# Optimization experiments

Hardware: AMD Instinct MI355X
Metric: run time of the kernel (lower is better)

The kernel has to match this reference:

```python
import jax, jax.numpy as jnp
import numpy as np

# 8 sign-flip operations: all combinations of (+-1, +-1, +-1), shape [8, 3]
OPS = jnp.array([[i, j, k] for i in (-1, 1) for j in (-1, 1) for k in (-1, 1)],
                dtype=jnp.float32)


def setup_inputs() -> dict:
    key = jax.random.key(0)
    k1, k2 = jax.random.split(key)
    B, N = 256, 4096
    X = jax.random.normal(k1, (B, N, 3), dtype=jnp.float32)
    mask = jnp.ones((B, N), dtype=jnp.float32)
    return {"X": X, "mask": mask}


def reference(X, mask):
    # X: [B, N, 3], mask: [B, N]
    m = mask[..., None]                                   # [B, N, 1]
    center = (X * m).sum(axis=1) / m.sum(axis=1)          # [B, 3]
    # torch: X = X - center.unsqueeze(1) * mask  (subtract center only where masked)
    Xc = X - center[:, None, :] * m                       # [B, N, 3]
    # 3x3 covariance per batch element
    C = jnp.einsum('bpi,bpj->bij', Xc, Xc)                # [B, 3, 3]
    # eigh on detached covariance (no grad through eigendecomposition)
    L, V = jnp.linalg.eigh(jax.lax.stop_gradient(C))      # V: [B, 3, 3]
    # F_ops[b,o,i,j] = ops[o,j] * V[b,i,j]  -> [B, 8, 3, 3]
    F_ops = OPS[None, :, None, :] * V[:, None, :, :]
    # h[b,o,p,i] = sum_j F_ops[b,o,j,i] * Xc[b,p,j]
    h = jnp.einsum('boji,bpj->bopi', F_ops, Xc)           # [B, 8, N, 3]
    h = h.reshape(X.shape[0] * 8, X.shape[1], 3)          # [B*8, N, 3]
    return h, jax.lax.stop_gradient(F_ops), center
```

## Files before the change

kernel.cpp:

```cpp
#include <hip/hip_runtime.h>
#include <math.h>

#ifndef USE_NEW_LARTG
#define USE_NEW_LARTG 1
#endif

#define BB 256
#define NN 4096


__device__ __forceinline__ float ssign_(float a, float b) {
  return (b >= 0.0f) ? fabsf(a) : -fabsf(a);
}

__device__ __forceinline__ float slapy2f_(float x, float y) {
#pragma clang fp contract(off)
  float xa = fabsf(x), ya = fabsf(y);
  float w = fmaxf(xa, ya), z = fminf(xa, ya);
  if (z == 0.0f) return w;
  float q = z / w;
  return w * __fsqrt_rn(1.0f + q * q);
}

__device__ __forceinline__ void slartgf_(float f, float g, float& cs, float& sn, float& r) {
#pragma clang fp contract(off)
#if USE_NEW_LARTG
  if (g == 0.0f) { cs = 1.0f; sn = 0.0f; r = f; }
  else if (f == 0.0f) { cs = 0.0f; sn = (g >= 0.0f) ? 1.0f : -1.0f; r = fabsf(g); }
  else {
    float d = __fsqrt_rn(f * f + g * g);
    cs = fabsf(f) / d;
    r = ssign_(d, f);
    sn = g / r;
  }
#else
  if (g == 0.0f) { cs = 1.0f; sn = 0.0f; r = f; }
  else if (f == 0.0f) { cs = 0.0f; sn = 1.0f; r = g; }
  else {
    float rr = __fsqrt_rn(f * f + g * g);
    cs = f / rr;
    sn = g / rr;
    r = rr;
    if (fabsf(f) > fabsf(g) && cs < 0.0f) { cs = -cs; sn = -sn; r = -r; }
  }
#endif
}

__device__ void slaev2f_(float a, float b, float c, float& rt1, float& rt2,
                         float& cs1, float& sn1) {
#pragma clang fp contract(off)
  float sm = a + c;
  float df = a - c;
  float adf = fabsf(df);
  float tb = b + b;
  float ab = fabsf(tb);
  float acmx, acmn;
  if (fabsf(a) > fabsf(c)) { acmx = a; acmn = c; } else { acmx = c; acmn = a; }
  float rt;
  if (adf > ab)      { float q = ab / adf; rt = adf * __fsqrt_rn(1.0f + q * q); }
  else if (adf < ab) { float q = adf / ab; rt = ab * __fsqrt_rn(1.0f + q * q); }
  else               { rt = ab * __fsqrt_rn(2.0f); }
  int sgn1;
  if (sm < 0.0f)      { rt1 = 0.5f * (sm - rt); sgn1 = -1; rt2 = (acmx / rt1) * acmn - (b / rt1) * b; }
  else if (sm > 0.0f) { rt1 = 0.5f * (sm + rt); sgn1 = 1;  rt2 = (acmx / rt1) * acmn - (b / rt1) * b; }
  else                { rt1 = 0.5f * rt; rt2 = -0.5f * rt; sgn1 = 1; }
  float cs;
  int sgn2;
  if (df >= 0.0f) { cs = df + rt; sgn2 = 1; } else { cs = df - rt; sgn2 = -1; }
  float acs = fabsf(cs);
  if (acs > ab) {
    float ct = -tb / cs;
    sn1 = 1.0f / __fsqrt_rn(1.0f + ct * ct);
    cs1 = ct * sn1;
  } else {
    if (ab == 0.0f) { cs1 = 1.0f; sn1 = 0.0f; }
    else { float tn = -cs / tb; cs1 = 1.0f / __fsqrt_rn(1.0f + tn * tn); sn1 = tn * cs1; }
  }
  if (sgn1 == sgn2) { float tn = cs1; cs1 = -sn1; sn1 = tn; }
}

__device__ void steqr3f_(float* d, float* e, float z[4][4]) {
#pragma clang fp contract(off)
  const float eps = 5.9604645e-08f;
  const float eps2 = eps * eps;
  const float safmin = 1.17549435e-38f;
  const int n = 3, nm1 = 2, nmaxit = 3 * 30;
  int jtot = 0, l1 = 1;
  int l, m, lsv, lend, lendsv, i, j, ii, k;
  float p, g, r, c, s, f, b, rt1, rt2, tst, anorm, temp, cj, sj;
  float wc[3], ws_[3];
  wc[0] = wc[1] = wc[2] = 0.0f; ws_[0] = ws_[1] = ws_[2] = 0.0f;

L10:
  if (l1 > n) goto L160;
  if (l1 > 1) e[l1 - 1] = 0.0f;
  if (l1 <= nm1) {
    for (m = l1; m <= nm1; ++m) {
      tst = fabsf(e[m]);
      if (tst == 0.0f) goto L30;
      if (tst <= (__fsqrt_rn(fabsf(d[m])) * __fsqrt_rn(fabsf(d[m + 1]))) * eps) {
        e[m] = 0.0f; goto L30;
      }
    }
  }
  m = n;
L30:
  l = l1; lsv = l; lend = m; lendsv = lend; l1 = m + 1;
  if (lend == l) goto L10;
  anorm = 0.0f;
  for (i = l; i <= lend; ++i) anorm = fmaxf(anorm, fabsf(d[i]));
  for (i = l; i <= lend - 1; ++i) anorm = fmaxf(anorm, fabsf(e[i]));
  if (anorm == 0.0f) goto L10;
  if (fabsf(d[lend]) < fabsf(d[l])) { lend = lsv; l = lendsv; }

  if (lend > l) {
L40:
    if (l != lend) {
      for (m = l; m <= lend - 1; ++m) {
        tst = e[m] * e[m];
        if (tst <= (eps2 * fabsf(d[m])) * fabsf(d[m + 1]) + safmin) goto L60;
      }
    }
    m = lend;
L60:
    if (m < lend) e[m] = 0.0f;
    p = d[l];
    if (m == l) goto L80;
    if (m == l + 1) {
      slaev2f_(d[l], e[l], d[l + 1], rt1, rt2, c, s);
      wc[l] = c; ws_[l] = s;
      for (i = 1; i <= 3; ++i) {
        temp = z[i][l + 1];
        z[i][l + 1] = c * temp - s * z[i][l];
        z[i][l]     = s * temp + c * z[i][l];
      }
      d[l] = rt1; d[l + 1] = rt2; e[l] = 0.0f;
      l = l + 2;
      if (l <= lend) goto L40;
      goto L140;
    }
    if (jtot == nmaxit) goto L140;
    jtot = jtot + 1;
    g = (d[l + 1] - p) / (2.0f * e[l]);
    r = slapy2f_(g, 1.0f);
    g = d[m] - p + e[l] / (g + ssign_(r, g));
    s = 1.0f; c = 1.0f; p = 0.0f;
    for (i = m - 1; i >= l; --i) {
      f = s * e[i]; b = c * e[i];
      slartgf_(g, f, c, s, r);
      if (i != m - 1) e[i + 1] = r;
      g = d[i + 1] - p;
      r = (d[i] - g) * s + 2.0f * c * b;
      p = s * r;
      d[i + 1] = g + p;
      g = c * r - b;
      wc[i] = c; ws_[i] = -s;
    }
    for (j = (m - l + 1) - 1; j >= 1; --j) {
      cj = wc[l + j - 1]; sj = ws_[l + j - 1];
      for (i = 1; i <= 3; ++i) {
        temp = z[i][l + j];
        z[i][l + j]     = cj * temp - sj * z[i][l + j - 1];
        z[i][l + j - 1] = sj * temp + cj * z[i][l + j - 1];
      }
    }
    d[l] = d[l] - p;
    e[l] = g;
    goto L40;
L80:
    d[l] = p;
    l = l + 1;
    if (l <= lend) goto L40;
    goto L140;
  } else {
L90:
    if (l != lend) {
      for (m = l; m >= lend + 1; --m) {
        tst = e[m - 1] * e[m - 1];
        if (tst <= (eps2 * fabsf(d[m])) * fabsf(d[m - 1]) + safmin) goto L110;
      }
    }
    m = lend;
L110:
    if (m > lend) e[m - 1] = 0.0f;
    p = d[l];
    if (m == l) goto L130;
    if (m == l - 1) {
      slaev2f_(d[l - 1], e[l - 1], d[l], rt1, rt2, c, s);
      wc[m] = c; ws_[m] = s;
      for (i = 1; i <= 3; ++i) {
        temp = z[i][l];
        z[i][l]     = c * temp - s * z[i][l - 1];
        z[i][l - 1] = s * temp + c * z[i][l - 1];
      }
      d[l - 1] = rt1; d[l] = rt2; e[l - 1] = 0.0f;
      l = l - 2;
      if (l >= lend) goto L90;
      goto L140;
    }
    if (jtot == nmaxit) goto L140;
    jtot = jtot + 1;
    g = (d[l - 1] - p) / (2.0f * e[l - 1]);
    r = slapy2f_(g, 1.0f);
    g = d[m] - p + e[l - 1] / (g + ssign_(r, g));
    s = 1.0f; c = 1.0f; p = 0.0f;
    for (i = m; i <= l - 1; ++i) {
      f = s * e[i]; b = c * e[i];
      slartgf_(g, f, c, s, r);
      if (i != m) e[i - 1] = r;
      g = d[i] - p;
      r = (d[i + 1] - g) * s + 2.0f * c * b;
      p = s * r;
      d[i] = g + p;
      g = c * r - b;
      wc[i] = c; ws_[i] = s;
    }
    for (j = 1; j <= (l - m + 1) - 1; ++j) {
      cj = wc[m + j - 1]; sj = ws_[m + j - 1];
      for (i = 1; i <= 3; ++i) {
        temp = z[i][m + j];
        z[i][m + j]     = cj * temp - sj * z[i][m + j - 1];
        z[i][m + j - 1] = sj * temp + cj * z[i][m + j - 1];
      }
    }
    d[l] = d[l] - p;
    e[l - 1] = g;
    goto L90;
L130:
    d[l] = p;
    l = l - 1;
    if (l >= lend) goto L90;
    goto L140;
  }
L140:
  if (jtot < nmaxit) goto L10;
  goto L190;
L160:
  for (ii = 2; ii <= n; ++ii) {
    i = ii - 1; k = i; p = d[i];
    for (j = ii; j <= n; ++j) {
      if (d[j] < p) { k = j; p = d[j]; }
    }
    if (k != i) {
      d[k] = d[i]; d[i] = p;
      for (int q = 1; q <= 3; ++q) { temp = z[q][i]; z[q][i] = z[q][k]; z[q][k] = temp; }
    }
  }
L190:
  return;
}

__device__ void eigh3f_(const float C[3][3], float V[3][3]) {
#pragma clang fp contract(off)
  float a11 = C[0][0], a21 = C[1][0], a31 = C[2][0];
  float a22 = C[1][1], a32 = C[2][1], a33 = C[2][2];
  float d[4], e[3], tau1, v3;
  float xnorm = fabsf(a31);
  if (xnorm == 0.0f) {
    tau1 = 0.0f; v3 = 0.0f;
    d[1] = a11; d[2] = a22; d[3] = a33; e[1] = a21; e[2] = a32;
  } else {
    float beta = -ssign_(slapy2f_(a21, xnorm), a21);
    tau1 = (beta - a21) / beta;
    v3 = a31 / (a21 - beta);
    e[1] = beta;
    float x1 = tau1 * a22 + tau1 * (a32 * v3);
    float x2 = tau1 * a32 + (tau1 * v3) * a33;
    float al = -0.5f * tau1 * (x1 + x2 * v3);
    float w1 = x1 + al;
    float w2 = x2 + al * v3;
    d[1] = a11;
    d[2] = (a22 - w1) - w1;
    e[2] = (a32 - v3 * w1) - w2;
    d[3] = (a33 - v3 * w2) - w2 * v3;
  }
  float z[4][4];
  for (int i = 1; i <= 3; ++i)
    for (int j = 1; j <= 3; ++j) z[i][j] = (i == j) ? 1.0f : 0.0f;
  steqr3f_(d, e, z);
  if (tau1 != 0.0f) {
    for (int j = 1; j <= 3; ++j) {
      float wj = z[2][j] + z[3][j] * v3;
      float tmp = -(tau1 * wj);
      z[2][j] = z[2][j] + tmp;
      z[3][j] = z[3][j] + v3 * tmp;
    }
  }
  for (int i = 0; i < 3; ++i)
    for (int j = 0; j < 3; ++j) V[i][j] = z[i + 1][j + 1];
}

__global__ __launch_bounds__(256) void k_stats_eigh(
    const float* __restrict__ X, const float* __restrict__ mask,
    float* __restrict__ out_fops, float* __restrict__ out_center,
    float* __restrict__ ws) {
  int b = blockIdx.x;
  int t = threadIdx.x;
  const float4* Xv = reinterpret_cast<const float4*>(X);
  const float4* Mv = reinterpret_cast<const float4*>(mask);

  double acc[11];
  for (int q = 0; q < 11; ++q) acc[q] = 0.0;
  for (int kk = 0; kk < 4; ++kk) {
    int fi = b * 3072 + kk * 768 + 3 * t;
    float4 v0 = Xv[fi], v1 = Xv[fi + 1], v2 = Xv[fi + 2];
    float4 mm = Mv[b * 1024 + kk * 256 + t];
    float px[4] = {v0.x, v0.w, v1.z, v2.y};
    float py[4] = {v0.y, v1.x, v1.w, v2.z};
    float pz[4] = {v0.z, v1.y, v2.x, v2.w};
    float pm[4] = {mm.x, mm.y, mm.z, mm.w};
#pragma unroll
    for (int q = 0; q < 4; ++q) {
      double x = px[q], y = py[q], zz = pz[q], m = pm[q];
      acc[0] += m;       acc[1] += m * m;
      acc[2] += m * x;   acc[3] += m * y;   acc[4] += m * zz;
      acc[5] += x * x;   acc[6] += x * y;   acc[7] += x * zz;
      acc[8] += y * y;   acc[9] += y * zz;  acc[10] += zz * zz;
    }
  }
#pragma unroll
  for (int off = 32; off > 0; off >>= 1)
    for (int q = 0; q < 11; ++q) acc[q] += __shfl_down(acc[q], off, 64);

  __shared__ double sh[4][11];
  int wid = t >> 6, lane = t & 63;
  if (lane == 0)
    for (int q = 0; q < 11; ++q) sh[wid][q] = acc[q];
  __syncthreads();

  if (t == 0) {
    double r[11];
    for (int q = 0; q < 11; ++q) r[q] = sh[0][q] + sh[1][q] + sh[2][q] + sh[3][q];
    double W = r[0], W2 = r[1];
    double ssum[3] = {r[2], r[3], r[4]};
    double M[3][3] = {{r[5], r[6], r[7]}, {r[6], r[8], r[9]}, {r[7], r[9], r[10]}};
    double cc[3] = {ssum[0] / W, ssum[1] / W, ssum[2] / W};
    float Cf[3][3];
    for (int i = 0; i < 3; ++i)
      for (int j = 0; j < 3; ++j)
        Cf[i][j] = (float)(M[i][j] - (ssum[i] * cc[j] + cc[i] * ssum[j]) + W2 * cc[i] * cc[j]);
    float Vf[3][3];
    eigh3f_(Cf, Vf);
    float cf[3] = {(float)cc[0], (float)cc[1], (float)cc[2]};
    float* wb = ws + b * 12;
    for (int i = 0; i < 3; ++i)
      for (int j = 0; j < 3; ++j) wb[i * 3 + j] = Vf[i][j];
    wb[9] = cf[0]; wb[10] = cf[1]; wb[11] = cf[2];
    out_center[b * 3 + 0] = cf[0];
    out_center[b * 3 + 1] = cf[1];
    out_center[b * 3 + 2] = cf[2];
    for (int o = 0; o < 8; ++o) {
      float sgn[3] = {(o & 4) ? 1.f : -1.f, (o & 2) ? 1.f : -1.f, (o & 1) ? 1.f : -1.f};
      for (int i = 0; i < 3; ++i)
        for (int j = 0; j < 3; ++j)
          out_fops[b * 72 + o * 9 + i * 3 + j] = sgn[j] * Vf[i][j];
    }
  }
}

__global__ __launch_bounds__(256) void k_apply(
    const float* __restrict__ X, const float* __restrict__ mask,
    const float* __restrict__ ws, float* __restrict__ h) {
  int blk = blockIdx.x;
  int b = blk >> 2;
  int chunk = blk & 3;
  int t = threadIdx.x;

  const float* wb = ws + b * 12;
  float V0 = wb[0], V1 = wb[1], V2 = wb[2];
  float V3 = wb[3], V4 = wb[4], V5 = wb[5];
  float V6 = wb[6], V7 = wb[7], V8 = wb[8];
  float c0 = wb[9], c1 = wb[10], c2 = wb[11];

  const float4* Xv = reinterpret_cast<const float4*>(X);
  int fi = b * 3072 + chunk * 768 + 3 * t;
  float4 v0 = Xv[fi], v1 = Xv[fi + 1], v2 = Xv[fi + 2];
  float4 mm = reinterpret_cast<const float4*>(mask)[b * 1024 + chunk * 256 + t];
  float px[4] = {v0.x, v0.w, v1.z, v2.y};
  float py[4] = {v0.y, v1.x, v1.w, v2.z};
  float pz[4] = {v0.z, v1.y, v2.x, v2.w};
  float pm[4] = {mm.x, mm.y, mm.z, mm.w};

  float ya[4], yb[4], yc[4];
#pragma unroll
  for (int q = 0; q < 4; ++q) {
    float xcx = px[q] - c0 * pm[q];
    float xcy = py[q] - c1 * pm[q];
    float xcz = pz[q] - c2 * pm[q];
    ya[q] = V0 * xcx + V3 * xcy + V6 * xcz;
    yb[q] = V1 * xcx + V4 * xcy + V7 * xcz;
    yc[q] = V2 * xcx + V5 * xcy + V8 * xcz;
  }

  __shared__ float ylds[3072];
  float4* yv = reinterpret_cast<float4*>(ylds);
  yv[3 * t]     = make_float4(ya[0], yb[0], yc[0], ya[1]);
  yv[3 * t + 1] = make_float4(yb[1], yc[1], ya[2], yb[2]);
  yv[3 * t + 2] = make_float4(yc[2], ya[3], yb[3], yc[3]);
  __syncthreads();

  uint4 r0 = reinterpret_cast<const uint4*>(ylds)[t];
  uint4 r1 = reinterpret_cast<const uint4*>(ylds)[t + 256];
  uint4 r2 = reinterpret_cast<const uint4*>(ylds)[t + 512];

  int c0i = t % 3;
  int c1i = c0i + 1; if (c1i == 3) c1i = 0;
  int c2i = c1i + 1; if (c2i == 3) c2i = 0;

  uint4* hv = reinterpret_cast<uint4*>(h);
  int hb = 3072 * (b * 8) + 768 * chunk;
#pragma unroll
  for (int o = 0; o < 8; ++o) {
    unsigned s0 = (o & 4) ? 0u : 0x80000000u;
    unsigned s1 = (o & 2) ? 0u : 0x80000000u;
    unsigned s2 = (o & 1) ? 0u : 0x80000000u;
    unsigned sg[3] = {s0, s1, s2};
    uint4 m0 = make_uint4(sg[c0i], sg[c1i], sg[c2i], sg[c0i]);
    uint4 m1 = make_uint4(sg[c1i], sg[c2i], sg[c0i], sg[c1i]);
    uint4 m2 = make_uint4(sg[c2i], sg[c0i], sg[c1i], sg[c2i]);
    int base = hb + 3072 * o;
    hv[base + t]       = make_uint4(r0.x ^ m0.x, r0.y ^ m0.y, r0.z ^ m0.z, r0.w ^ m0.w);
    hv[base + t + 256] = make_uint4(r1.x ^ m1.x, r1.y ^ m1.y, r1.z ^ m1.z, r1.w ^ m1.w);
    hv[base + t + 512] = make_uint4(r2.x ^ m2.x, r2.y ^ m2.y, r2.z ^ m2.z, r2.w ^ m2.w);
  }
}

extern "C" void kernel_launch(void* const* d_in, const int* in_sizes, int n_in,
                              void* d_out, int out_size, void* d_ws, size_t ws_size,
                              hipStream_t stream) {
  const float* X = (const float*)d_in[0];
  const float* mask = (const float*)d_in[1];
  float* out = (float*)d_out;
  float* h = out;
  float* fops = out + (size_t)BB * 8 * NN * 3;
  float* center = fops + (size_t)BB * 8 * 9;
  float* ws = (float*)d_ws;

  hipLaunchKernelGGL(k_stats_eigh, dim3(BB), dim3(256), 0, stream,
                     X, mask, fops, center, ws);
  hipLaunchKernelGGL(k_apply, dim3(BB * 4), dim3(256), 0, stream,
                     X, mask, ws, h);
}
```

Measured before the change: 37.27 us.

## Split stats reduction across four blocks per batch and fold eigh into apply

The statistics kernel now launches four blocks per batch element, each reducing a quarter of the points into double partial sums in workspace, instead of one block looping over all points. The apply kernel sums the four partials, and its thread 0 runs the 3x3 eigensolver, sharing V and the center with the block through shared memory. This spreads the reduction over more CUs and removes the serial eigh tail from the first kernel. In exchange the eigh is computed redundantly in four blocks per batch, and every apply block stalls on a single thread's eigensolve before it can write output.

```diff
diff --git a/kernel.cpp b/kernel.cpp
--- a/kernel.cpp
+++ b/kernel.cpp
@@ -290,36 +290,37 @@
     for (int j = 0; j < 3; ++j) V[i][j] = z[i + 1][j + 1];
 }
 
-__global__ __launch_bounds__(256) void k_stats_eigh(
+__global__ __launch_bounds__(256, 4) void k_part(
     const float* __restrict__ X, const float* __restrict__ mask,
-    float* __restrict__ out_fops, float* __restrict__ out_center,
-    float* __restrict__ ws) {
-  int b = blockIdx.x;
+    double* __restrict__ wpart) {
+  int blk = blockIdx.x;
+  int b = blk >> 2;
+  int chunk = blk & 3;
   int t = threadIdx.x;
+
   const float4* Xv = reinterpret_cast<const float4*>(X);
-  const float4* Mv = reinterpret_cast<const float4*>(mask);
+  int fi = b * 3072 + chunk * 768 + 3 * t;
+  float4 v0 = Xv[fi], v1 = Xv[fi + 1], v2 = Xv[fi + 2];
+  float4 mm = reinterpret_cast<const float4*>(mask)[b * 1024 + chunk * 256 + t];
+  float px[4] = {v0.x, v0.w, v1.z, v2.y};
+  float py[4] = {v0.y, v1.x, v1.w, v2.z};
+  float pz[4] = {v0.z, v1.y, v2.x, v2.w};
+  float pm[4] = {mm.x, mm.y, mm.z, mm.w};
 
   double acc[11];
+#pragma unroll
   for (int q = 0; q < 11; ++q) acc[q] = 0.0;
-  for (int kk = 0; kk < 4; ++kk) {
-    int fi = b * 3072 + kk * 768 + 3 * t;
-    float4 v0 = Xv[fi], v1 = Xv[fi + 1], v2 = Xv[fi + 2];
-    float4 mm = Mv[b * 1024 + kk * 256 + t];
-    float px[4] = {v0.x, v0.w, v1.z, v2.y};
-    float py[4] = {v0.y, v1.x, v1.w, v2.z};
-    float pz[4] = {v0.z, v1.y, v2.x, v2.w};
-    float pm[4] = {mm.x, mm.y, mm.z, mm.w};
-#pragma unroll
-    for (int q = 0; q < 4; ++q) {
-      double x = px[q], y = py[q], zz = pz[q], m = pm[q];
-      acc[0] += m;       acc[1] += m * m;
-      acc[2] += m * x;   acc[3] += m * y;   acc[4] += m * zz;
-      acc[5] += x * x;   acc[6] += x * y;   acc[7] += x * zz;
-      acc[8] += y * y;   acc[9] += y * zz;  acc[10] += zz * zz;
-    }
+#pragma unroll
+  for (int q = 0; q < 4; ++q) {
+    double x = px[q], y = py[q], zz = pz[q], m = pm[q];
+    acc[0] += m;       acc[1] += m * m;
+    acc[2] += m * x;   acc[3] += m * y;   acc[4] += m * zz;
+    acc[5] += x * x;   acc[6] += x * y;   acc[7] += x * zz;
+    acc[8] += y * y;   acc[9] += y * zz;  acc[10] += zz * zz;
   }
 #pragma unroll
   for (int off = 32; off > 0; off >>= 1)
+#pragma unroll
     for (int q = 0; q < 11; ++q) acc[q] += __shfl_down(acc[q], off, 64);
 
   __shared__ double sh[4][11];
@@ -327,10 +328,34 @@
   if (lane == 0)
     for (int q = 0; q < 11; ++q) sh[wid][q] = acc[q];
   __syncthreads();
-
   if (t == 0) {
+    double* wp = wpart + (size_t)blk * 11;
+    for (int q = 0; q < 11; ++q)
+      wp[q] = sh[0][q] + sh[1][q] + sh[2][q] + sh[3][q];
+  }
+}
+
+__global__ __launch_bounds__(256, 4) void k_apply2(
+    const float* __restrict__ X, const float* __restrict__ mask,
+    const double* __restrict__ wpart,
+    float* __restrict__ out_fops, float* __restrict__ out_center,
+    float* __restrict__ h) {
+  int blk = blockIdx.x;
+  int b = blk >> 2;
+  int chunk = blk & 3;
+  int t = threadIdx.x;
+
+  const float4* Xv = reinterpret_cast<const float4*>(X);
+  int fi = b * 3072 + chunk * 768 + 3 * t;
+  float4 v0 = Xv[fi], v1 = Xv[fi + 1], v2 = Xv[fi + 2];
+  float4 mm = reinterpret_cast<const float4*>(mask)[b * 1024 + chunk * 256 + t];
+
+  __shared__ float svc[12];
+  if (t == 0) {
+    const double* base = wpart + (size_t)(b * 4) * 11;
     double r[11];
-    for (int q = 0; q < 11; ++q) r[q] = sh[0][q] + sh[1][q] + sh[2][q] + sh[3][q];
+    for (int q = 0; q < 11; ++q)
+      r[q] = base[q] + base[11 + q] + base[22 + q] + base[33 + q];
     double W = r[0], W2 = r[1];
     double ssum[3] = {r[2], r[3], r[4]};
     double M[3][3] = {{r[5], r[6], r[7]}, {r[6], r[8], r[9]}, {r[7], r[9], r[10]}};
@@ -342,40 +367,28 @@
     float Vf[3][3];
     eigh3f_(Cf, Vf);
     float cf[3] = {(float)cc[0], (float)cc[1], (float)cc[2]};
-    float* wb = ws + b * 12;
     for (int i = 0; i < 3; ++i)
-      for (int j = 0; j < 3; ++j) wb[i * 3 + j] = Vf[i][j];
-    wb[9] = cf[0]; wb[10] = cf[1]; wb[11] = cf[2];
-    out_center[b * 3 + 0] = cf[0];
-    out_center[b * 3 + 1] = cf[1];
-    out_center[b * 3 + 2] = cf[2];
-    for (int o = 0; o < 8; ++o) {
-      float sgn[3] = {(o & 4) ? 1.f : -1.f, (o & 2) ? 1.f : -1.f, (o & 1) ? 1.f : -1.f};
-      for (int i = 0; i < 3; ++i)
-        for (int j = 0; j < 3; ++j)
-          out_fops[b * 72 + o * 9 + i * 3 + j] = sgn[j] * Vf[i][j];
-    }
-  }
-}
-
-__global__ __launch_bounds__(256) void k_apply(
-    const float* __restrict__ X, const float* __restrict__ mask,
-    const float* __restrict__ ws, float* __restrict__ h) {
-  int blk = blockIdx.x;
-  int b = blk >> 2;
-  int chunk = blk & 3;
-  int t = threadIdx.x;
-
-  const float* wb = ws + b * 12;
-  float V0 = wb[0], V1 = wb[1], V2 = wb[2];
-  float V3 = wb[3], V4 = wb[4], V5 = wb[5];
-  float V6 = wb[6], V7 = wb[7], V8 = wb[8];
-  float c0 = wb[9], c1 = wb[10], c2 = wb[11];
-
-  const float4* Xv = reinterpret_cast<const float4*>(X);
-  int fi = b * 3072 + chunk * 768 + 3 * t;
-  float4 v0 = Xv[fi], v1 = Xv[fi + 1], v2 = Xv[fi + 2];
-  float4 mm = reinterpret_cast<const float4*>(mask)[b * 1024 + chunk * 256 + t];
+      for (int j = 0; j < 3; ++j) svc[i * 3 + j] = Vf[i][j];
+    svc[9] = cf[0]; svc[10] = cf[1]; svc[11] = cf[2];
+    if (chunk == 0) {
+      out_center[b * 3 + 0] = cf[0];
+      out_center[b * 3 + 1] = cf[1];
+      out_center[b * 3 + 2] = cf[2];
+      for (int o = 0; o < 8; ++o) {
+        float sgn[3] = {(o & 4) ? 1.f : -1.f, (o & 2) ? 1.f : -1.f, (o & 1) ? 1.f : -1.f};
+        for (int i = 0; i < 3; ++i)
+          for (int j = 0; j < 3; ++j)
+            out_fops[b * 72 + o * 9 + i * 3 + j] = sgn[j] * Vf[i][j];
+      }
+    }
+  }
+  __syncthreads();
+
+  float V0 = svc[0], V1 = svc[1], V2 = svc[2];
+  float V3 = svc[3], V4 = svc[4], V5 = svc[5];
+  float V6 = svc[6], V7 = svc[7], V8 = svc[8];
+  float c0 = svc[9], c1 = svc[10], c2 = svc[11];
+
   float px[4] = {v0.x, v0.w, v1.z, v2.y};
   float py[4] = {v0.y, v1.x, v1.w, v2.z};
   float pz[4] = {v0.z, v1.y, v2.x, v2.w};
@@ -434,10 +447,9 @@
   float* h = out;
   float* fops = out + (size_t)BB * 8 * NN * 3;
   float* center = fops + (size_t)BB * 8 * 9;
-  float* ws = (float*)d_ws;
-
-  hipLaunchKernelGGL(k_stats_eigh, dim3(BB), dim3(256), 0, stream,
-                     X, mask, fops, center, ws);
-  hipLaunchKernelGGL(k_apply, dim3(BB * 4), dim3(256), 0, stream,
-                     X, mask, ws, h);
-}
+  double* wpart = (double*)d_ws;
+
+  hipLaunchKernelGGL(k_part, dim3(BB * 4), dim3(256), 0, stream, X, mask, wpart);
+  hipLaunchKernelGGL(k_apply2, dim3(BB * 4), dim3(256), 0, stream,
+                     X, mask, wpart, fops, center, h);
+}
```

Result: no change. 38.00 us (+2.0%).
